# Optimization experiments

Measured on AMD Instinct MI355X. Metric: run time of the kernel, lower is better.

The kernel has to match this reference:

```python
import jax, jax.numpy as jnp
import numpy as np

B, T, D = 2, 4096, 1024      # batch, seq, hidden_dim
E, I = 16, 512               # n_routed_experts, expert_intermediate
K = 2                        # n_activated_experts
IS = 2048                    # shared_expert_intermediate
ALPHA = 1e-4                 # balance_loss_alpha
EPS = 1e-9


def setup_inputs() -> dict:
    key = jax.random.key(0)
    ks = jax.random.split(key, 8)
    s = lambda k, shape, fan: jax.random.normal(k, shape, jnp.float32) * (fan ** -0.5)
    return {
        "x": jax.random.normal(ks[0], (B, T, D), jnp.float32),
        "gate_w": s(ks[1], (D, E), D),            # router gate (no bias)
        "expert_bias": jnp.zeros((E,), jnp.float32),
        "sh_gate": s(ks[2], (D, IS), D),          # shared expert SwiGLU
        "sh_up": s(ks[3], (D, IS), D),
        "sh_down": s(ks[4], (IS, D), IS),
        "ex_gate": s(ks[5], (E, D, I), D),        # routed experts (stacked)
        "ex_up": s(ks[6], (E, D, I), D),
        "ex_down": s(ks[7], (E, I, D), I),
    }


def _swiglu(x, wg, wu, wd):
    return (jax.nn.silu(x @ wg) * (x @ wu)) @ wd


def reference(x, gate_w, expert_bias, sh_gate, sh_up, sh_down, ex_gate, ex_up, ex_down):
    Bq, Tq, Dq = x.shape
    # shared expert path (n_shared_experts = 1)
    shared = _swiglu(x, sh_gate, sh_up, sh_down)

    xf = x.reshape(Bq * Tq, Dq)                       # (N, D)
    N = xf.shape[0]

    # --- router: sigmoid gating, bias-adjusted top-k, normalized gates ---
    affinity = jax.nn.sigmoid(xf @ gate_w)            # (N, E)
    scores = affinity + expert_bias[None, :]
    _, idx = jax.lax.top_k(scores, K)                 # (N, K) int
    gv = jnp.take_along_axis(affinity, idx, axis=1)   # (N, K) gathered from affinity
    gv = gv / (gv.sum(-1, keepdims=True) + EPS)

    # --- balance loss (sequence-wise, Eq. 17-20) ---
    expert_mask = jax.nn.one_hot(idx, E, dtype=jnp.float32).sum(1)  # (N, E)
    f = expert_mask.sum(0) * E / (K * N)
    P = (affinity / (affinity.sum(-1, keepdims=True) + EPS)).mean(0)
    balance_loss = ALPHA * (f * P).sum()
    expert_counts = expert_mask.sum(0).astype(jnp.int32)            # (E,)

    # --- dispatch/compute/combine, expressed as dense combine-weight matrix ---
    # w[n, e] = sum of gate values for token n routed to expert e (same math
    # as the masked gather/scatter loop in the original)
    w = jnp.zeros((N, E), jnp.float32).at[jnp.arange(N)[:, None], idx].add(gv)
    h = jax.nn.silu(jnp.einsum('nd,edi->eni', xf, ex_gate)) \
        * jnp.einsum('nd,edi->eni', xf, ex_up)        # (E, N, I)
    routed = jnp.einsum('ne,eni,eid->nd', w, h, ex_down)  # (N, D)
    routed = routed.reshape(Bq, Tq, Dq)

    output = shared + routed  # note: original does NOT add residual despite docstring
    return output, balance_loss, expert_counts
```

## Files before the change

### kernel.cpp

```cpp
#include <hip/hip_runtime.h>
#include <stdint.h>

#define NTOK 8192
#define DDIM 1024
#define NEXP 16
#define KSEL 2
#define ISH 2048
#define IEX 512
#define ALPHAC 1e-4f
#define REPS 1e-9f

typedef __attribute__((ext_vector_type(8))) short short8;
typedef __attribute__((ext_vector_type(4))) float f32x4;

__device__ __forceinline__ unsigned short f2bf(float f){
  union { float f; uint32_t u; } v; v.f = f;
  uint32_t u = v.u;
  uint32_t r = (u + 0x7fffu + ((u >> 16) & 1u)) >> 16;
  return (unsigned short)r;
}
__device__ __forceinline__ float bf2f(unsigned short h){
  union { uint32_t u; float f; } v; v.u = ((uint32_t)h) << 16; return v.f;
}

__device__ __forceinline__ void gload16(const void* g, void* l){
  __builtin_amdgcn_global_load_lds(
      (const __attribute__((address_space(1))) void*)g,
      (__attribute__((address_space(3))) void*)l, 16, 0, 0);
}

__global__ __launch_bounds__(256) void convert_f32_bf16(const float* __restrict__ in,
                                                        unsigned short* __restrict__ out){
  int id = blockIdx.x * 256 + threadIdx.x;
  float4 v = ((const float4*)in)[id];
  ushort4 o;
  o.x = f2bf(v.x); o.y = f2bf(v.y); o.z = f2bf(v.z); o.w = f2bf(v.w);
  ((ushort4*)out)[id] = o;
}

template<int RM, int RO>
__global__ __launch_bounds__(256) void transpose_bf16(const float* __restrict__ in,
                                                      unsigned short* __restrict__ outp,
                                                      int R, int C){
  __shared__ float tile[64][65];
  const float* ip = in + (size_t)blockIdx.z * R * C;
  unsigned short* op = outp + (size_t)blockIdx.z * R * C * RM;
  int c0 = blockIdx.x * 64, r0 = blockIdx.y * 64;
  int t = threadIdx.x;
  int tr = t >> 4, tc = (t & 15) * 4;
  #pragma unroll
  for (int i = 0; i < 4; ++i){
    float4 v = *(const float4*)&ip[(size_t)(r0 + tr + i*16) * C + c0 + tc];
    tile[tr + i*16][tc+0] = v.x;
    tile[tr + i*16][tc+1] = v.y;
    tile[tr + i*16][tc+2] = v.z;
    tile[tr + i*16][tc+3] = v.w;
  }
  __syncthreads();
  #pragma unroll
  for (int i = 0; i < 4; ++i){
    int oc = tr + i*16;
    ushort4 w;
    w.x = f2bf(tile[tc+0][oc]);
    w.y = f2bf(tile[tc+1][oc]);
    w.z = f2bf(tile[tc+2][oc]);
    w.w = f2bf(tile[tc+3][oc]);
    *(ushort4*)&op[(size_t)((c0 + oc) * RM + RO) * R + r0 + tc] = w;
  }
}

__global__ __launch_bounds__(256) void logits_kernel(
    const float* __restrict__ x, const float* __restrict__ gw,
    float* __restrict__ logits)
{
  __shared__ float gws[16][1024];
  const int t = threadIdx.x;
  #pragma unroll
  for (int k = 0; k < 16; ++k){
    int idx = t + k * 256;
    float4 v = ((const float4*)gw)[idx];
    int d = idx >> 2, e0 = (idx & 3) * 4;
    gws[e0+0][d] = v.x;
    gws[e0+1][d] = v.y;
    gws[e0+2][d] = v.z;
    gws[e0+3][d] = v.w;
  }
  __syncthreads();
  const int lane = t & 63, w = t >> 6;
  const int nb = blockIdx.x * 16 + w * 4;
  for (int i = 0; i < 4; ++i){
    const int n = nb + i;
    const float4* xr = (const float4*)(x + (size_t)n * DDIM);
    float4 xv[4];
    #pragma unroll
    for (int k = 0; k < 4; ++k) xv[k] = xr[lane + k*64];
    float acc[16];
    #pragma unroll
    for (int e = 0; e < 16; ++e){
      float s = 0.f;
      #pragma unroll
      for (int k = 0; k < 4; ++k){
        float4 g = *(const float4*)&gws[e][(lane + k*64)*4];
        s = fmaf(xv[k].x, g.x, fmaf(xv[k].y, g.y, fmaf(xv[k].z, g.z, fmaf(xv[k].w, g.w, s))));
      }
      acc[e] = s;
    }
    #pragma unroll
    for (int m = 1; m < 64; m <<= 1)
      #pragma unroll
      for (int e = 0; e < 16; ++e)
        acc[e] += __shfl_xor(acc[e], m);
    if (lane == 0){
      float4* op = (float4*)(logits + (size_t)n * 16);
      op[0] = make_float4(acc[0],  acc[1],  acc[2],  acc[3]);
      op[1] = make_float4(acc[4],  acc[5],  acc[6],  acc[7]);
      op[2] = make_float4(acc[8],  acc[9],  acc[10], acc[11]);
      op[3] = make_float4(acc[12], acc[13], acc[14], acc[15]);
    }
  }
}

__global__ __launch_bounds__(256) void router_finish(
    const float* __restrict__ logits, const float* __restrict__ ebias,
    int* __restrict__ idxb, float* __restrict__ gvb,
    float* __restrict__ Ppart, int* __restrict__ Cpart)
{
  __shared__ float Ps[16];
  __shared__ int Cs[16];
  const int t = threadIdx.x;
  if (t < 16){ Ps[t] = 0.f; Cs[t] = 0; }
  __syncthreads();
  const int lane = t & 63;
  const int n = blockIdx.x * 256 + t;
  const float4* lp = (const float4*)(logits + (size_t)n * 16);
  float4 a0 = lp[0], a1 = lp[1], a2 = lp[2], a3 = lp[3];
  float aff[16];
  aff[0]=a0.x; aff[1]=a0.y; aff[2]=a0.z; aff[3]=a0.w;
  aff[4]=a1.x; aff[5]=a1.y; aff[6]=a1.z; aff[7]=a1.w;
  aff[8]=a2.x; aff[9]=a2.y; aff[10]=a2.z; aff[11]=a2.w;
  aff[12]=a3.x; aff[13]=a3.y; aff[14]=a3.z; aff[15]=a3.w;
  float rowsum = REPS;
  #pragma unroll
  for (int e = 0; e < 16; ++e){
    aff[e] = 1.f / (1.f + __expf(-aff[e]));
    rowsum += aff[e];
  }
  float bj[16];
  #pragma unroll
  for (int e = 0; e < 16; ++e) bj[e] = ebias[e];
  float bestS = aff[0] + bj[0], bestA = aff[0]; int i1 = 0;
  #pragma unroll
  for (int j = 1; j < 16; ++j){
    float sc = aff[j] + bj[j];
    bool gt2 = sc > bestS;
    bestS = gt2 ? sc : bestS; bestA = gt2 ? aff[j] : bestA; i1 = gt2 ? j : i1;
  }
  float secS = -1e30f, secA = 0.f; int i2 = 0;
  #pragma unroll
  for (int j = 0; j < 16; ++j){
    float sc = aff[j] + bj[j];
    bool ok = (j != i1) && (sc > secS);
    secS = ok ? sc : secS; secA = ok ? aff[j] : secA; i2 = ok ? j : i2;
  }
  float den = bestA + secA + REPS;
  idxb[n*2]   = i1; idxb[n*2+1] = i2;
  gvb[n*2]    = bestA / den; gvb[n*2+1] = secA / den;

  float inv = 1.f / rowsum;
  float pv[16]; int cv[16];
  #pragma unroll
  for (int e = 0; e < 16; ++e){
    pv[e] = aff[e] * inv;
    cv[e] = (e == i1) + (e == i2);
  }
  #pragma unroll
  for (int m = 1; m < 64; m <<= 1)
    #pragma unroll
    for (int e = 0; e < 16; ++e){
      pv[e] += __shfl_xor(pv[e], m);
      cv[e] += __shfl_xor(cv[e], m);
    }
  if (lane == 0){
    #pragma unroll
    for (int e = 0; e < 16; ++e){
      atomicAdd(&Ps[e], pv[e]);
      atomicAdd(&Cs[e], cv[e]);
    }
  }
  __syncthreads();
  if (t < 16){ Ppart[blockIdx.x*16 + t] = Ps[t]; Cpart[blockIdx.x*16 + t] = Cs[t]; }
}

__global__ __launch_bounds__(256) void finalize2(
    const float* __restrict__ Ppart, const int* __restrict__ Cpart,
    int* __restrict__ counts, int* __restrict__ offs, int* __restrict__ cursor,
    float* __restrict__ out_tail)
{
  __shared__ float P[16];
  __shared__ int C[16];
  int t = threadIdx.x;
  if (t < 16){ P[t] = 0.f; C[t] = 0; }
  __syncthreads();
  if (t < 32){
    int e = t & 15, c = t >> 4;
    float p = 0.f; int cc = 0;
    for (int b = c * 16; b < c * 16 + 16; ++b){ p += Ppart[b*16 + e]; cc += Cpart[b*16 + e]; }
    atomicAdd(&P[e], p); atomicAdd(&C[e], cc);
  }
  __syncthreads();
  if (t == 0){
    int a = 0; float loss = 0.f;
    for (int i = 0; i < 16; ++i){
      offs[i] = a; cursor[i] = a; counts[i] = C[i]; a += C[i];
      loss += ((float)C[i] * (float)NEXP / (float)(KSEL * NTOK)) * (P[i] / (float)NTOK);
      out_tail[1+i] = (float)C[i];
    }
    out_tail[0] = ALPHAC * loss;
  }
}

__global__ __launch_bounds__(256) void slot_assign(
    const int* __restrict__ idxb, const float* __restrict__ gvb,
    int* __restrict__ cursor, int* __restrict__ tokp, float* __restrict__ gatep,
    int* __restrict__ rslot)
{
  int i = blockIdx.x * 256 + threadIdx.x;
  int e = idxb[i];
  int s = atomicAdd(&cursor[e], 1);
  tokp[s] = i >> 1;
  gatep[s] = gvb[i];
  rslot[i] = s;
}

template<bool GROUPED, bool GATHER, int MODE, int NYT>
__global__ __launch_bounds__(512, 1) void gemm256(
    const unsigned short* __restrict__ A,
    const unsigned short* __restrict__ B,
    void* __restrict__ Cout,
    int M, int N, int K,
    const int* __restrict__ counts,
    const int* __restrict__ offsets,
    const int* __restrict__ perm,
    const float* __restrict__ rowscale)
{
  __shared__ __align__(16) unsigned short As[2][256*64];
  __shared__ __align__(16) unsigned short Bs[2][256*64];

  const int nwg = gridDim.x;
  const int bid = blockIdx.x;
  const int wg = (bid & 7) * (nwg >> 3) + (bid >> 3);
  const int mtl = wg / NYT;
  const int ntc = wg % NYT;

  int mt = mtl, off = 0, cnt = M;
  const unsigned short* bp = B;
  if (GROUPED){
    int acc_ = 0, e = -1;
    #pragma unroll
    for (int i = 0; i < NEXP; ++i){
      int c = counts[i]; int tt = (c + 255) >> 8;
      if (e < 0 && mtl < acc_ + tt){ e = i; mt = mtl - acc_; off = offsets[i]; cnt = c; }
      acc_ += tt;
    }
    if (e < 0) return;
    bp += (size_t)e * N * K;
  }
  const int m0 = mt * 256, n0 = ntc * 256;
  const int t = threadIdx.x;
  const int lane = t & 63;
  const int wid = t >> 6;
  const int wm0 = (wid >> 2) * 128;
  const int wn0 = (wid & 3) * 64;
  const int l15 = lane & 15, g = lane >> 4;

  const unsigned short* asrc[4];
  const unsigned short* bsrc[4];
  int ldst[4];
  #pragma unroll
  for (int c = 0; c < 4; ++c){
    int slot = c * 512 + t;
    int row = slot >> 3, c16 = slot & 7;
    int scol = (c16 ^ (row & 7)) * 8;
    ldst[c] = slot * 8;
    int r = m0 + row;
    int rc = GROUPED ? (r < cnt ? r : (cnt > 0 ? cnt - 1 : 0)) : r;
    int ar;
    if (GATHER) ar = perm[off + rc];
    else        ar = GROUPED ? off + rc : rc;
    asrc[c] = A + (size_t)ar * K + scol;
    bsrc[c] = bp + (size_t)(n0 + row) * K + scol;
  }

  f32x4 acc[8][4];
  #pragma unroll
  for (int i = 0; i < 8; ++i)
    #pragma unroll
    for (int j = 0; j < 4; ++j)
      #pragma unroll
      for (int r = 0; r < 4; ++r) acc[i][j][r] = 0.f;

  auto STAGE = [&](int buf, int kt){
    const int k0 = kt << 6;
    #pragma unroll
    for (int c = 0; c < 4; ++c) gload16(asrc[c] + k0, (void*)&As[buf][ldst[c]]);
    #pragma unroll
    for (int c = 0; c < 4; ++c) gload16(bsrc[c] + k0, (void*)&Bs[buf][ldst[c]]);
  };

  const int ntk = K >> 6;
  STAGE(0, 0);
  __syncthreads();
  int cur = 0;
  for (int tk = 0; tk < ntk; ++tk){
    if (tk + 1 < ntk) STAGE(cur ^ 1, tk + 1);
    short8 bfr[4][2];
    #pragma unroll
    for (int j = 0; j < 4; ++j)
      #pragma unroll
      for (int ks = 0; ks < 2; ++ks){
        int row = wn0 + j * 16 + l15;
        bfr[j][ks] = *(const short8*)&Bs[cur][row * 64 + (((ks*4 + g) ^ (row & 7)) * 8)];
      }
    #pragma unroll
    for (int mi = 0; mi < 8; ++mi){
      int row = wm0 + mi * 16 + l15;
      short8 af0 = *(const short8*)&As[cur][row * 64 + (((0 + g) ^ (row & 7)) * 8)];
      short8 af1 = *(const short8*)&As[cur][row * 64 + (((4 + g) ^ (row & 7)) * 8)];
      #pragma unroll
      for (int j = 0; j < 4; ++j)
        acc[mi][j] = __builtin_amdgcn_mfma_f32_16x16x32_bf16(af0, bfr[j][0], acc[mi][j], 0, 0, 0);
      #pragma unroll
      for (int j = 0; j < 4; ++j)
        acc[mi][j] = __builtin_amdgcn_mfma_f32_16x16x32_bf16(af1, bfr[j][1], acc[mi][j], 0, 0, 0);
    }
    __syncthreads();
    cur ^= 1;
  }

  #pragma unroll
  for (int mi = 0; mi < 8; ++mi)
    #pragma unroll
    for (int j = 0; j < 4; ++j)
      #pragma unroll
      for (int r = 0; r < 4; ++r){
        int lr = wm0 + mi * 16 + g * 4 + r;
        int grow = m0 + lr;
        if (GROUPED && grow >= cnt) continue;
        int gcol = n0 + wn0 + j * 16 + l15;
        size_t orow = GROUPED ? (size_t)(off + grow) : (size_t)grow;
        float val = acc[mi][j][r];
        if (MODE == 1){
          ((float*)Cout)[orow * N + gcol] = val;
        } else if (MODE == 6){
          float uo = __shfl_xor(val, 1);
          if (!(l15 & 1)){
            float rv = val / (1.f + __expf(-val)) * uo;
            ((unsigned short*)Cout)[orow * (N >> 1) + (gcol >> 1)] = f2bf(rv);
          }
        } else {
          val *= rowscale[off + grow];
          ((unsigned short*)Cout)[orow * N + gcol] = f2bf(val);
        }
      }
}

__global__ __launch_bounds__(256) void combine_kernel(float* __restrict__ out,
                                                      const unsigned short* __restrict__ ybuf,
                                                      const int* __restrict__ rs){
  int id = blockIdx.x * 256 + threadIdx.x;
  int n = id >> 8;
  int q = id & 255;
  int s0 = rs[n*2], s1 = rs[n*2+1];
  float4 o = ((float4*)out)[id];
  ushort4 a = ((const ushort4*)(ybuf + (size_t)s0 * DDIM))[q];
  ushort4 b = ((const ushort4*)(ybuf + (size_t)s1 * DDIM))[q];
  o.x += bf2f(a.x) + bf2f(b.x);
  o.y += bf2f(a.y) + bf2f(b.y);
  o.z += bf2f(a.z) + bf2f(b.z);
  o.w += bf2f(a.w) + bf2f(b.w);
  ((float4*)out)[id] = o;
}

extern "C" void kernel_launch(void* const* d_in, const int* in_sizes, int n_in,
                              void* d_out, int out_size, void* d_ws, size_t ws_size,
                              hipStream_t stream)
{
  const float* x       = (const float*)d_in[0];
  const float* gate_w  = (const float*)d_in[1];
  const float* ebias   = (const float*)d_in[2];
  const float* sh_gate = (const float*)d_in[3];
  const float* sh_up   = (const float*)d_in[4];
  const float* sh_down = (const float*)d_in[5];
  const float* ex_gate = (const float*)d_in[6];
  const float* ex_up   = (const float*)d_in[7];
  const float* ex_down = (const float*)d_in[8];
  float* out = (float*)d_out;
  (void)in_sizes; (void)n_in; (void)out_size; (void)ws_size;

  size_t o = 0;
  auto alloc = [&](size_t bytes) -> void* {
    o = (o + 255) & ~(size_t)255;
    void* p = (char*)d_ws + o;
    o += bytes;
    return p;
  };
  unsigned short* xb    = (unsigned short*)alloc((size_t)NTOK*DDIM*2);
  unsigned short* shguT = (unsigned short*)alloc((size_t)2*ISH*DDIM*2);
  unsigned short* shdT  = (unsigned short*)alloc((size_t)DDIM*ISH*2);
  unsigned short* exguT = (unsigned short*)alloc((size_t)NEXP*2*IEX*DDIM*2);
  unsigned short* exdT  = (unsigned short*)alloc((size_t)NEXP*DDIM*IEX*2);
  unsigned short* hbuf  = (unsigned short*)alloc((size_t)NTOK*KSEL*IEX*2);
  unsigned short* big   = (unsigned short*)alloc((size_t)NTOK*ISH*2);
  float* logits = (float*)alloc((size_t)NTOK*NEXP*4);
  int*   idxb  = (int*)alloc(NTOK*KSEL*4);
  float* gvb   = (float*)alloc(NTOK*KSEL*4);
  float* Ppart = (float*)alloc(32*16*4);
  int*   Cpart = (int*)alloc(32*16*4);
  int*   counts= (int*)alloc(64);
  int*   offs  = (int*)alloc(64);
  int*   cursor= (int*)alloc(64);
  int*   tokp  = (int*)alloc(NTOK*KSEL*4);
  float* gatep = (float*)alloc(NTOK*KSEL*4);
  int*   rslot = (int*)alloc(NTOK*KSEL*4);

  convert_f32_bf16<<<NTOK*DDIM/1024, 256, 0, stream>>>(x, xb);
  transpose_bf16<2,0><<<dim3(ISH/64,  DDIM/64, 1),    256, 0, stream>>>(sh_gate, shguT, DDIM, ISH);
  transpose_bf16<2,1><<<dim3(ISH/64,  DDIM/64, 1),    256, 0, stream>>>(sh_up,   shguT, DDIM, ISH);
  transpose_bf16<1,0><<<dim3(DDIM/64, ISH/64,  1),    256, 0, stream>>>(sh_down, shdT, ISH, DDIM);
  transpose_bf16<2,0><<<dim3(IEX/64,  DDIM/64, NEXP), 256, 0, stream>>>(ex_gate, exguT, DDIM, IEX);
  transpose_bf16<2,1><<<dim3(IEX/64,  DDIM/64, NEXP), 256, 0, stream>>>(ex_up,   exguT, DDIM, IEX);
  transpose_bf16<1,0><<<dim3(DDIM/64, IEX/64,  NEXP), 256, 0, stream>>>(ex_down, exdT, IEX, DDIM);

  logits_kernel<<<512, 256, 0, stream>>>(x, gate_w, logits);
  router_finish<<<32, 256, 0, stream>>>(logits, ebias, idxb, gvb, Ppart, Cpart);
  finalize2<<<1, 256, 0, stream>>>(Ppart, Cpart, counts, offs, cursor,
                                   out + (size_t)NTOK*DDIM);
  slot_assign<<<NTOK*KSEL/256, 256, 0, stream>>>(idxb, gvb, cursor, tokp, gatep, rslot);

  gemm256<false,false,6,16><<<32*16, 512, 0, stream>>>(
      xb, shguT, big, NTOK, 2*ISH, DDIM, nullptr, nullptr, nullptr, nullptr);
  gemm256<false,false,1,4><<<32*4, 512, 0, stream>>>(
      big, shdT, out, NTOK, DDIM, ISH, nullptr, nullptr, nullptr, nullptr);

  gemm256<true,true,6,4><<<80*4, 512, 0, stream>>>(
      xb, exguT, hbuf, 0, 2*IEX, DDIM, counts, offs, tokp, nullptr);
  gemm256<true,false,2,4><<<80*4, 512, 0, stream>>>(
      hbuf, exdT, big, 0, DDIM, IEX, counts, offs, nullptr, gatep);

  combine_kernel<<<NTOK*DDIM/1024, 256, 0, stream>>>(out, big, rslot);
}
```

Measured before the change: 457.3 us.

## Add 128x128 single-buffered GEMM for down-proj and grouped expert GEMMs

Adds a gemm128 kernel with 128x128 tiles, 256 threads and a single LDS buffer, and uses it for the shared down projection and both grouped routed-expert GEMMs. The 256x256 double-buffered kernel stays only for the large shared gate/up GEMM. Small tiles raise the workgroup count for the narrow-N GEMMs (128 to 512 blocks on the down projection) and cut padding waste in the grouped expert tiles. In exchange they lose compute reuse per tile and drop the prefetch overlap, so loads and MFMA no longer overlap within a block.

After: 398.3 us. 1.15x faster.

```diff
diff --git a/kernel.cpp b/kernel.cpp
--- a/kernel.cpp
+++ b/kernel.cpp
@@ -233,7 +233,7 @@
 }
 
 template<bool GROUPED, bool GATHER, int MODE, int NYT>
-__global__ __launch_bounds__(512, 1) void gemm256(
+__global__ __launch_bounds__(256) void gemm128(
     const unsigned short* __restrict__ A,
     const unsigned short* __restrict__ B,
     void* __restrict__ Cout,
@@ -243,14 +243,14 @@
     const int* __restrict__ perm,
     const float* __restrict__ rowscale)
 {
-  __shared__ __align__(16) unsigned short As[2][256*64];
-  __shared__ __align__(16) unsigned short Bs[2][256*64];
+  __shared__ __align__(16) unsigned short As[128*64];
+  __shared__ __align__(16) unsigned short Bs[128*64];
 
   const int nwg = gridDim.x;
   const int bid = blockIdx.x;
   const int wg = (bid & 7) * (nwg >> 3) + (bid >> 3);
   const int mtl = wg / NYT;
-  const int ntc = wg % NYT;
+  const int nt  = wg % NYT;
 
   int mt = mtl, off = 0, cnt = M;
   const unsigned short* bp = B;
@@ -258,30 +258,30 @@
     int acc_ = 0, e = -1;
     #pragma unroll
     for (int i = 0; i < NEXP; ++i){
-      int c = counts[i]; int tt = (c + 255) >> 8;
+      int c = counts[i]; int tt = (c + 127) >> 7;
       if (e < 0 && mtl < acc_ + tt){ e = i; mt = mtl - acc_; off = offsets[i]; cnt = c; }
       acc_ += tt;
     }
     if (e < 0) return;
     bp += (size_t)e * N * K;
   }
-  const int m0 = mt * 256, n0 = ntc * 256;
+  const int m0 = mt * 128, n0 = nt * 128;
   const int t = threadIdx.x;
   const int lane = t & 63;
   const int wid = t >> 6;
-  const int wm0 = (wid >> 2) * 128;
-  const int wn0 = (wid & 3) * 64;
+  const int wm = (wid >> 1) * 64;
+  const int wn = (wid & 1) * 64;
   const int l15 = lane & 15, g = lane >> 4;
 
   const unsigned short* asrc[4];
   const unsigned short* bsrc[4];
-  int ldst[4];
+  int ldso[4];
   #pragma unroll
   for (int c = 0; c < 4; ++c){
-    int slot = c * 512 + t;
-    int row = slot >> 3, c16 = slot & 7;
+    int s = (wid*4 + c)*64 + lane;
+    int row = s >> 3, c16 = s & 7;
     int scol = (c16 ^ (row & 7)) * 8;
-    ldst[c] = slot * 8;
+    ldso[c] = (wid*4 + c) * 512;
     int r = m0 + row;
     int rc = GROUPED ? (r < cnt ? r : (cnt > 0 ? cnt - 1 : 0)) : r;
     int ar;
@@ -291,64 +291,56 @@
     bsrc[c] = bp + (size_t)(n0 + row) * K + scol;
   }
 
-  f32x4 acc[8][4];
-  #pragma unroll
-  for (int i = 0; i < 8; ++i)
+  f32x4 acc[4][4];
+  #pragma unroll
+  for (int i = 0; i < 4; ++i)
     #pragma unroll
     for (int j = 0; j < 4; ++j)
       #pragma unroll
       for (int r = 0; r < 4; ++r) acc[i][j][r] = 0.f;
 
-  auto STAGE = [&](int buf, int kt){
-    const int k0 = kt << 6;
-    #pragma unroll
-    for (int c = 0; c < 4; ++c) gload16(asrc[c] + k0, (void*)&As[buf][ldst[c]]);
-    #pragma unroll
-    for (int c = 0; c < 4; ++c) gload16(bsrc[c] + k0, (void*)&Bs[buf][ldst[c]]);
-  };
-
   const int ntk = K >> 6;
-  STAGE(0, 0);
-  __syncthreads();
-  int cur = 0;
   for (int tk = 0; tk < ntk; ++tk){
-    if (tk + 1 < ntk) STAGE(cur ^ 1, tk + 1);
-    short8 bfr[4][2];
+    const int k0 = tk << 6;
+    #pragma unroll
+    for (int c = 0; c < 4; ++c) gload16(asrc[c] + k0, (void*)&As[ldso[c]]);
+    #pragma unroll
+    for (int c = 0; c < 4; ++c) gload16(bsrc[c] + k0, (void*)&Bs[ldso[c]]);
+    __syncthreads();
+    #pragma unroll
+    for (int ks = 0; ks < 2; ++ks){
+      short8 af[4], bf[4];
+      #pragma unroll
+      for (int i = 0; i < 4; ++i){
+        int row = wm + i * 16 + l15;
+        af[i] = *(const short8*)&As[row * 64 + (((ks*4 + g) ^ (row & 7)) * 8)];
+      }
+      #pragma unroll
+      for (int j = 0; j < 4; ++j){
+        int row = wn + j * 16 + l15;
+        bf[j] = *(const short8*)&Bs[row * 64 + (((ks*4 + g) ^ (row & 7)) * 8)];
+      }
+      #pragma unroll
+      for (int i = 0; i < 4; ++i)
+        #pragma unroll
+        for (int j = 0; j < 4; ++j)
+          acc[i][j] = __builtin_amdgcn_mfma_f32_16x16x32_bf16(af[i], bf[j], acc[i][j], 0, 0, 0);
+    }
+    __syncthreads();
+  }
+
+  #pragma unroll
+  for (int i = 0; i < 4; ++i)
     #pragma unroll
     for (int j = 0; j < 4; ++j)
       #pragma unroll
-      for (int ks = 0; ks < 2; ++ks){
-        int row = wn0 + j * 16 + l15;
-        bfr[j][ks] = *(const short8*)&Bs[cur][row * 64 + (((ks*4 + g) ^ (row & 7)) * 8)];
-      }
-    #pragma unroll
-    for (int mi = 0; mi < 8; ++mi){
-      int row = wm0 + mi * 16 + l15;
-      short8 af0 = *(const short8*)&As[cur][row * 64 + (((0 + g) ^ (row & 7)) * 8)];
-      short8 af1 = *(const short8*)&As[cur][row * 64 + (((4 + g) ^ (row & 7)) * 8)];
-      #pragma unroll
-      for (int j = 0; j < 4; ++j)
-        acc[mi][j] = __builtin_amdgcn_mfma_f32_16x16x32_bf16(af0, bfr[j][0], acc[mi][j], 0, 0, 0);
-      #pragma unroll
-      for (int j = 0; j < 4; ++j)
-        acc[mi][j] = __builtin_amdgcn_mfma_f32_16x16x32_bf16(af1, bfr[j][1], acc[mi][j], 0, 0, 0);
-    }
-    __syncthreads();
-    cur ^= 1;
-  }
-
-  #pragma unroll
-  for (int mi = 0; mi < 8; ++mi)
-    #pragma unroll
-    for (int j = 0; j < 4; ++j)
-      #pragma unroll
       for (int r = 0; r < 4; ++r){
-        int lr = wm0 + mi * 16 + g * 4 + r;
+        int lr = wm + i * 16 + g * 4 + r;
         int grow = m0 + lr;
         if (GROUPED && grow >= cnt) continue;
-        int gcol = n0 + wn0 + j * 16 + l15;
+        int gcol = n0 + wn + j * 16 + l15;
         size_t orow = GROUPED ? (size_t)(off + grow) : (size_t)grow;
-        float val = acc[mi][j][r];
+        float val = acc[i][j][r];
         if (MODE == 1){
           ((float*)Cout)[orow * N + gcol] = val;
         } else if (MODE == 6){
@@ -360,6 +352,111 @@
         } else {
           val *= rowscale[off + grow];
           ((unsigned short*)Cout)[orow * N + gcol] = f2bf(val);
+        }
+      }
+}
+
+template<int MODE, int NYT>
+__global__ __launch_bounds__(512, 1) void gemm256(
+    const unsigned short* __restrict__ A,
+    const unsigned short* __restrict__ B,
+    void* __restrict__ Cout,
+    int M, int N, int K)
+{
+  __shared__ __align__(16) unsigned short As[2][256*64];
+  __shared__ __align__(16) unsigned short Bs[2][256*64];
+
+  const int nwg = gridDim.x;
+  const int bid = blockIdx.x;
+  const int wg = (bid & 7) * (nwg >> 3) + (bid >> 3);
+  const int mt  = wg / NYT;
+  const int ntc = wg % NYT;
+
+  const int m0 = mt * 256, n0 = ntc * 256;
+  const int t = threadIdx.x;
+  const int lane = t & 63;
+  const int wid = t >> 6;
+  const int wm0 = (wid >> 2) * 128;
+  const int wn0 = (wid & 3) * 64;
+  const int l15 = lane & 15, g = lane >> 4;
+
+  const unsigned short* asrc[4];
+  const unsigned short* bsrc[4];
+  int ldst[4];
+  #pragma unroll
+  for (int c = 0; c < 4; ++c){
+    int slot = c * 512 + t;
+    int row = slot >> 3, c16 = slot & 7;
+    int scol = (c16 ^ (row & 7)) * 8;
+    ldst[c] = slot * 8;
+    asrc[c] = A + (size_t)(m0 + row) * K + scol;
+    bsrc[c] = B + (size_t)(n0 + row) * K + scol;
+  }
+
+  f32x4 acc[8][4];
+  #pragma unroll
+  for (int i = 0; i < 8; ++i)
+    #pragma unroll
+    for (int j = 0; j < 4; ++j)
+      #pragma unroll
+      for (int r = 0; r < 4; ++r) acc[i][j][r] = 0.f;
+
+  auto STAGE = [&](int buf, int kt){
+    const int k0 = kt << 6;
+    #pragma unroll
+    for (int c = 0; c < 4; ++c) gload16(asrc[c] + k0, (void*)&As[buf][ldst[c]]);
+    #pragma unroll
+    for (int c = 0; c < 4; ++c) gload16(bsrc[c] + k0, (void*)&Bs[buf][ldst[c]]);
+  };
+
+  const int ntk = K >> 6;
+  STAGE(0, 0);
+  __syncthreads();
+  int cur = 0;
+  for (int tk = 0; tk < ntk; ++tk){
+    if (tk + 1 < ntk) STAGE(cur ^ 1, tk + 1);
+    short8 bfr[4][2];
+    #pragma unroll
+    for (int j = 0; j < 4; ++j)
+      #pragma unroll
+      for (int ks = 0; ks < 2; ++ks){
+        int row = wn0 + j * 16 + l15;
+        bfr[j][ks] = *(const short8*)&Bs[cur][row * 64 + (((ks*4 + g) ^ (row & 7)) * 8)];
+      }
+    #pragma unroll
+    for (int mi = 0; mi < 8; ++mi){
+      int row = wm0 + mi * 16 + l15;
+      short8 af0 = *(const short8*)&As[cur][row * 64 + (((0 + g) ^ (row & 7)) * 8)];
+      short8 af1 = *(const short8*)&As[cur][row * 64 + (((4 + g) ^ (row & 7)) * 8)];
+      #pragma unroll
+      for (int j = 0; j < 4; ++j)
+        acc[mi][j] = __builtin_amdgcn_mfma_f32_16x16x32_bf16(af0, bfr[j][0], acc[mi][j], 0, 0, 0);
+      #pragma unroll
+      for (int j = 0; j < 4; ++j)
+        acc[mi][j] = __builtin_amdgcn_mfma_f32_16x16x32_bf16(af1, bfr[j][1], acc[mi][j], 0, 0, 0);
+    }
+    __syncthreads();
+    cur ^= 1;
+  }
+
+  #pragma unroll
+  for (int mi = 0; mi < 8; ++mi)
+    #pragma unroll
+    for (int j = 0; j < 4; ++j)
+      #pragma unroll
+      for (int r = 0; r < 4; ++r){
+        int lr = wm0 + mi * 16 + g * 4 + r;
+        int grow = m0 + lr;
+        int gcol = n0 + wn0 + j * 16 + l15;
+        float val = acc[mi][j][r];
+        if (MODE == 6){
+          float uo = __shfl_xor(val, 1);
+          if (!(l15 & 1)){
+            float rv = val / (1.f + __expf(-val)) * uo;
+            ((unsigned short*)Cout)[(size_t)grow * (N >> 1) + (gcol >> 1)] = f2bf(rv);
+          }
+        } else {
+          ((float*)Cout)[(size_t)grow * N + gcol] = val;
         }
       }
 }
@@ -437,14 +534,14 @@
                                    out + (size_t)NTOK*DDIM);
   slot_assign<<<NTOK*KSEL/256, 256, 0, stream>>>(idxb, gvb, cursor, tokp, gatep, rslot);
 
-  gemm256<false,false,6,16><<<32*16, 512, 0, stream>>>(
-      xb, shguT, big, NTOK, 2*ISH, DDIM, nullptr, nullptr, nullptr, nullptr);
-  gemm256<false,false,1,4><<<32*4, 512, 0, stream>>>(
+  gemm256<6,16><<<32*16, 512, 0, stream>>>(
+      xb, shguT, big, NTOK, 2*ISH, DDIM);
+  gemm128<false,false,1,8><<<64*8, 256, 0, stream>>>(
       big, shdT, out, NTOK, DDIM, ISH, nullptr, nullptr, nullptr, nullptr);
 
-  gemm256<true,true,6,4><<<80*4, 512, 0, stream>>>(
+  gemm128<true,true,6,8><<<144*8, 256, 0, stream>>>(
       xb, exguT, hbuf, 0, 2*IEX, DDIM, counts, offs, tokp, nullptr);
-  gemm256<true,false,2,4><<<80*4, 512, 0, stream>>>(
+  gemm128<true,false,2,8><<<144*8, 256, 0, stream>>>(
       hbuf, exdT, big, 0, DDIM, IEX, counts, offs, nullptr, gatep);
 
   combine_kernel<<<NTOK*DDIM/1024, 256, 0, stream>>>(out, big, rslot);
```
